# Performance work log

Measured on AMD Instinct MI355X. Metric: run time of the kernel, lower is better.

Reference implementation:

```python
import jax, jax.numpy as jnp
import numpy as np

B, V, H, W, CIN, COUT = 2, 4, 256, 256, 64, 64
WINDOW = 1
GAMMA = 0.1


def setup_inputs() -> dict:
    key = jax.random.key(0)
    ks = jax.random.split(key, 6)
    # gaussian positions: x,y in [-1,1], z in [0.5,2.5] so projection masks are nontrivial
    means = jax.random.uniform(ks[0], (B, V, H, W, 3), dtype=jnp.float32)
    means = means * jnp.array([2.0, 2.0, 2.0], jnp.float32) + jnp.array([-1.0, -1.0, 0.5], jnp.float32)
    depths = jax.random.uniform(ks[1], (B, V, H, W, 1, 1), dtype=jnp.float32)
    gs_feats = jax.random.normal(ks[2], (B, V, H, W, CIN), dtype=jnp.float32)
    # normalized intrinsics (ndc in [0,1))
    intr = jnp.array([[0.8, 0.0, 0.5], [0.0, 0.8, 0.5], [0.0, 0.0, 1.0]], jnp.float32)
    intrinsics = jnp.broadcast_to(intr, (B, V, 3, 3))
    # camera-to-world extrinsics: identity rotation, small per-view translations
    t = jax.random.uniform(ks[3], (B, V, 3), minval=-0.2, maxval=0.2, dtype=jnp.float32)
    extrinsics = jnp.broadcast_to(jnp.eye(4, dtype=jnp.float32), (B, V, 4, 4)).at[..., :3, 3].set(t)
    w1 = jax.random.normal(ks[4], (COUT, CIN, 3, 3), dtype=jnp.float32) * 0.05
    b1 = jnp.zeros((COUT,), jnp.float32)
    w2 = jax.random.normal(ks[5], (COUT, COUT, 3, 3), dtype=jnp.float32) * 0.05
    b2 = jnp.zeros((COUT,), jnp.float32)
    return {"means": means, "depths": depths, "gs_feats": gs_feats,
            "intrinsics": intrinsics, "extrinsics": extrinsics,
            "w1": w1, "b1": b1, "w2": w2, "b2": b2}


def _project(points, intr, extr, eps=1e-8):
    # points (b, n, 3) world; extr (b,4,4) cam-to-world; intr (b,3,3) normalized
    w2c = jnp.linalg.inv(extr)
    ph = jnp.concatenate([points, jnp.ones_like(points[..., :1])], axis=-1)  # (b,n,4)
    cam = jnp.einsum('bij,bnj->bni', w2c, ph)[..., :3]
    z = cam[..., 2:3]
    ndc = jnp.einsum('bij,bnj->bni', intr, cam / (z + eps))
    return ndc[..., :2], cam[..., 2] > eps


def _conv3x3(x, w, b):
    y = jax.lax.conv_general_dilated(x, w, (1, 1), 'SAME',
                                     dimension_numbers=('NCHW', 'OIHW', 'NCHW'))
    return y + b[None, :, None, None]


def reference(means, depths, gs_feats, intrinsics, extrinsics, w1, b1, w2, b2):
    b, v, h, w_, c = gs_feats.shape
    hw = h * w_
    feats_flat = gs_feats.reshape(b, v, hw, c)
    pts = means.reshape(b, v, hw, 3)
    outs = []
    for j in range(v):
        acc = feats_flat[:, j]                      # (b, hw, c)
        norm = jnp.ones((b,), gs_feats.dtype)
        for k in range(v):
            if j != k and (k - WINDOW) <= j <= (k + WINDOW):
                ndc, valid_z = _project(pts[:, j], intrinsics[:, k], extrinsics[:, k])
                px = jnp.floor(ndc[..., 0] * w_).astype(jnp.int32)
                py = jnp.floor(ndc[..., 1] * h).astype(jnp.int32)
                mask = ((ndc[..., 0] >= 0) & (ndc[..., 0] < 1) &
                        (ndc[..., 1] >= 0) & (ndc[..., 1] < 1) & valid_z)  # (b,hw)
                idx = jnp.clip(py, 0, h - 1) * w_ + jnp.clip(px, 0, w_ - 1)
                gathered = jnp.take_along_axis(feats_flat[:, k], idx[..., None], axis=1)
                upd = jnp.where(mask[..., None], gathered, jnp.zeros((), gs_feats.dtype))
                scale = GAMMA * mask.sum(-1).astype(gs_feats.dtype) / (h * w_)  # (b,)
                acc = acc + upd * scale[:, None, None]
                norm = norm + scale
        outs.append(acc / norm[:, None, None])
    fused = jnp.stack(outs, axis=1).reshape(b * v, h, w_, c).transpose(0, 3, 1, 2)  # (bv,c,h,w)
    x = _conv3x3(fused, w1, b1)
    x = jax.nn.gelu(x, approximate=False)
    x = _conv3x3(x, w2, b2)
    return x.transpose(0, 2, 3, 1).reshape(b, v, h, w_, -1)
```

## Files before the change

kernel.cpp:

```cpp
#include <hip/hip_runtime.h>
#include <math.h>

#define HW 65536
#define NPAD 258

typedef short bf16x8 __attribute__((ext_vector_type(8)));
typedef float f32x4  __attribute__((ext_vector_type(4)));

#define O_COUNTS 0
#define O_W2C    2048
#define O_WT     4096
#define O_META   151552
#define O_FUSED  3297280
#define O_X1     71458816

#define HROWB   4224
#define HROWSTR 4240
#define HBUF    25440

__device__ __forceinline__ unsigned short f2bf(float f) {
    unsigned int u = __float_as_uint(f);
    u += 0x7FFFu + ((u >> 16) & 1u);
    return (unsigned short)(u >> 16);
}

__device__ __forceinline__ unsigned int cvt_pk_bf16(float lo, float hi) {
    unsigned int r;
    asm("v_cvt_pk_bf16_f32 %0, %1, %2" : "=v"(r) : "v"(lo), "v"(hi));
    return r;
}

__device__ __forceinline__ float gelu_fast(float v) {
    float x  = v * 0.70710678118654752f;
    float ax = fabsf(x);
    float t  = __builtin_amdgcn_rcpf(fmaf(0.3275911f, ax, 1.0f));
    float p  = fmaf(t, 1.061405429f, -1.453152027f);
    p = fmaf(t, p, 1.421413741f);
    p = fmaf(t, p, -0.284496736f);
    p = fmaf(t, p, 0.254829592f);
    p = p * t;
    float e   = __expf(-x * x);
    float era = fmaf(-p, e, 1.0f);
    float er  = copysignf(era, x);
    return 0.5f * v * (1.0f + er);
}

__global__ __launch_bounds__(256) void prep_kernel(
    const float* __restrict__ extr, const float* __restrict__ w1,
    const float* __restrict__ w2, float* __restrict__ w2c,
    unsigned short* __restrict__ wT, unsigned short* __restrict__ fusedP,
    unsigned short* __restrict__ x1P, int* __restrict__ counts)
{
    int tid = blockIdx.x * blockDim.x + threadIdx.x;
    int nth = gridDim.x * blockDim.x;

    if (blockIdx.x == 0) {
        if (threadIdx.x < 8) {
            float a[4][8];
            const float* E = extr + threadIdx.x * 16;
            for (int r = 0; r < 4; r++)
                for (int c = 0; c < 4; c++) {
                    a[r][c] = E[r*4 + c];
                    a[r][4+c] = (r == c) ? 1.0f : 0.0f;
                }
            for (int col = 0; col < 4; col++) {
                int piv = col; float bm = fabsf(a[col][col]);
                for (int r = col+1; r < 4; r++) {
                    float v = fabsf(a[r][col]);
                    if (v > bm) { bm = v; piv = r; }
                }
                if (piv != col)
                    for (int c = 0; c < 8; c++) { float t = a[col][c]; a[col][c] = a[piv][c]; a[piv][c] = t; }
                float f = 1.0f / a[col][col];
                for (int c = 0; c < 8; c++) a[col][c] *= f;
                for (int r = 0; r < 4; r++) if (r != col) {
                    float f2 = a[r][col];
                    for (int c = 0; c < 8; c++) a[r][c] -= f2 * a[col][c];
                }
            }
            float* O = w2c + threadIdx.x * 16;
            for (int r = 0; r < 4; r++)
                for (int c = 0; c < 4; c++) O[r*4+c] = a[r][4+c];
        }
    }

    for (int i = tid; i < 384; i += nth) counts[i] = 0;

    for (int e = tid; e < 73728; e += nth) {
        int t = e;
        int j  = t & 7;  t >>= 3;
        int co = t & 63; t >>= 6;
        int q  = t & 3;  t >>= 2;
        int tap = t % 9; t /= 9;
        int h  = t & 1;  int cv = t >> 1;
        int ci = h*32 + q*8 + j;
        int ky = tap / 3, kx = tap % 3;
        const float* wsrc = cv ? w2 : w1;
        float v = wsrc[((co*64 + ci)*3 + ky)*3 + kx];
        wT[cv*36864 + ((((h*9 + tap)*4 + q)*64 + co)*8 + j)] = f2bf(v);
    }

    for (int u = tid; u < 2*8*1028*8; u += nth) {
        int t = u;
        int ch   = t & 7;    t >>= 3;
        int cell = t % 1028; t /= 1028;
        int n    = t & 7;    int buf = t >> 3;
        int y, x;
        if      (cell < 258) { y = 0;   x = cell; }
        else if (cell < 516) { y = 257; x = cell - 258; }
        else if (cell < 772) { y = cell - 516 + 1; x = 0; }
        else                 { y = cell - 772 + 1; x = 257; }
        unsigned short* p = (buf ? x1P : fusedP) +
            (((size_t)(n*NPAD + y)*NPAD + x)*64 + ch*8);
        *reinterpret_cast<uint4*>(p) = make_uint4(0u, 0u, 0u, 0u);
    }
}

__global__ __launch_bounds__(256) void proj_kernel(
    const float* __restrict__ means, const float* __restrict__ intr,
    const float* __restrict__ w2c, int* __restrict__ meta,
    int* __restrict__ counts)
{
    const int jt[6] = {0,1,1,2,2,3};
    const int kt[6] = {1,0,2,1,3,2};
    int s = blockIdx.y;
    int b = s / 6, p = s % 6;
    int j = jt[p], k = kt[p];
    int i = blockIdx.x * 256 + threadIdx.x;

    __shared__ int bcnt;
    if (threadIdx.x == 0) bcnt = 0;
    __syncthreads();

    const float* mp = means + ((size_t)(b*4 + j)*HW + i)*3;
    float x = mp[0], y = mp[1], z = mp[2];
    const float* M = w2c + (b*4 + k)*16;
    const float* I = intr + (b*4 + k)*9;

    float cx = fmaf(M[2],  z, fmaf(M[1], y, M[0]*x)) + M[3];
    float cy = fmaf(M[6],  z, fmaf(M[5], y, M[4]*x)) + M[7];
    float cz = fmaf(M[10], z, fmaf(M[9], y, M[8]*x)) + M[11];

    bool vz = cz > 1e-8f;
    float zi = cz + 1e-8f;
    float sx = cx / zi, sy = cy / zi, sz = cz / zi;
    float nx = fmaf(I[2], sz, fmaf(I[1], sy, I[0]*sx));
    float ny = fmaf(I[5], sz, fmaf(I[4], sy, I[3]*sx));

    int px = (int)floorf(nx * 256.0f);
    int py = (int)floorf(ny * 256.0f);
    bool mask = (nx >= 0.0f) && (nx < 1.0f) && (ny >= 0.0f) && (ny < 1.0f) && vz;
    int pxc = min(max(px, 0), 255);
    int pyc = min(max(py, 0), 255);
    int idx = pyc*256 + pxc;
    meta[(size_t)s*HW + i] = idx | (mask ? (int)0x80000000 : 0);

    unsigned long long bal = __ballot(mask ? 1 : 0);
    if ((threadIdx.x & 63) == 0)
        atomicAdd(&bcnt, (int)__popcll(bal));
    __syncthreads();
    if (threadIdx.x == 0)
        atomicAdd(counts + s*32, bcnt);
}

__global__ __launch_bounds__(256) void fuse_kernel(
    const float* __restrict__ feats, const int* __restrict__ meta,
    const int* __restrict__ counts, unsigned short* __restrict__ fusedP)
{
    const int nsl[4]    = {1, 2, 2, 1};
    const int slt[4][2] = {{0,0},{1,2},{3,4},{5,5}};
    const int kvw[4][2] = {{1,1},{0,2},{1,3},{2,2}};

    int bj = blockIdx.y;
    int b = bj >> 2, j = bj & 3;
    int base = blockIdx.x * 32;
    int cg = threadIdx.x & 15;
    int pt0 = base + (threadIdx.x >> 4);
    int pt1 = pt0 + 16;

    int ns = nsl[j];

    const float4* fj0 = reinterpret_cast<const float4*>(
        feats + ((size_t)bj*HW + pt0)*64) + cg;
    const float4* fj1 = reinterpret_cast<const float4*>(
        feats + ((size_t)bj*HW + pt1)*64) + cg;
    float4 acc0 = *fj0;
    float4 acc1 = *fj1;
    float norm = 1.0f;

#pragma unroll
    for (int e = 0; e < 2; e++) {
        if (e < ns) {
            int p = slt[j][e], k = kvw[j][e];
            int s = b*6 + p;
            float scale = 0.1f * (float)counts[s*32] / 65536.0f;
            int mt0 = meta[(size_t)s*HW + pt0];
            int mt1 = meta[(size_t)s*HW + pt1];
            const float* fk = feats + (size_t)(b*4 + k)*HW*64;
            float4 g0 = *(reinterpret_cast<const float4*>(
                fk + (size_t)(mt0 & 0xFFFF)*64) + cg);
            float4 g1 = *(reinterpret_cast<const float4*>(
                fk + (size_t)(mt1 & 0xFFFF)*64) + cg);
            float w0 = (mt0 < 0) ? scale : 0.0f;
            float w1 = (mt1 < 0) ? scale : 0.0f;
            acc0.x = fmaf(w0, g0.x, acc0.x); acc0.y = fmaf(w0, g0.y, acc0.y);
            acc0.z = fmaf(w0, g0.z, acc0.z); acc0.w = fmaf(w0, g0.w, acc0.w);
            acc1.x = fmaf(w1, g1.x, acc1.x); acc1.y = fmaf(w1, g1.y, acc1.y);
            acc1.z = fmaf(w1, g1.z, acc1.z); acc1.w = fmaf(w1, g1.w, acc1.w);
            norm += scale;
        }
    }
    float rn = 1.0f / norm;

    int yy0 = pt0 >> 8, xx0 = pt0 & 255;
    unsigned short* op0 = fusedP +
        (((size_t)bj*NPAD + (yy0+1))*NPAD + (xx0+1))*64 + cg*4;
    *reinterpret_cast<uint2*>(op0) =
        make_uint2(cvt_pk_bf16(acc0.x*rn, acc0.y*rn),
                   cvt_pk_bf16(acc0.z*rn, acc0.w*rn));

    int yy1 = pt1 >> 8, xx1 = pt1 & 255;
    unsigned short* op1 = fusedP +
        (((size_t)bj*NPAD + (yy1+1))*NPAD + (xx1+1))*64 + cg*4;
    *reinterpret_cast<uint2*>(op1) =
        make_uint2(cvt_pk_bf16(acc1.x*rn, acc1.y*rn),
                   cvt_pk_bf16(acc1.z*rn, acc1.w*rn));
}

template<int MODE>
__global__ __launch_bounds__(256) void conv_kernel(
    const unsigned short* __restrict__ in, const unsigned short* __restrict__ wT,
    const float* __restrict__ bias, void* __restrict__ outp)
{
    __shared__ unsigned short smem[2 * HBUF / 2];

    int fid = blockIdx.x;
    int n   = fid & 7;
    int rem = fid >> 3;
    int y0  = (rem >> 2) << 2;
    int X0  = (rem & 3) << 6;

    int w  = threadIdx.x >> 6;
    int lane = threadIdx.x & 63;
    int m = lane & 15, q = lane >> 4;

    int srcl = ((lane >> 2) * 128) + ((((lane & 3) ^ ((lane >> 3) & 3)) & 3) << 4);
    int tsrcl = 8192 + ((lane >> 2) * 128) + ((lane & 3) << 4);

    int vb[3];
#pragma unroll
    for (int dx = 0; dx < 3; dx++)
        vb[dx] = w*HROWSTR + m*64 + (((q ^ (((m + dx) >> 1) & 3)) & 3) << 4);

    int wvoff = q*1024 + m*16;

    const char* gb00 = (const char*)in +
        (((size_t)(n*NPAD) + y0) * NPAD + X0) * 128;

    auto STAGE = [&](int row128, int h, int buf) {
        const char* gb = gb00 + (size_t)row128 * (NPAD*128) + h*64;
        char* lb = (char*)smem + buf*HBUF;
        for (int ri = w; ri < 6; ri += 4) {
            const char* g = gb + (size_t)ri * (NPAD*128);
            char* l = lb + ri*HROWSTR;
#pragma unroll
            for (int i = 0; i < 4; i++)
                __builtin_amdgcn_global_load_lds(
                    (const __attribute__((address_space(1))) unsigned int*)(g + i*2048 + srcl),
                    (__attribute__((address_space(3))) unsigned int*)(l + i*1024 + (size_t)lane*16),
                    16, 0, 0);
            if (lane < 8)
                __builtin_amdgcn_global_load_lds(
                    (const __attribute__((address_space(1))) unsigned int*)(g + tsrcl),
                    (__attribute__((address_space(3))) unsigned int*)(l + 4096 + (size_t)lane*16),
                    16, 0, 0);
        }
    };

    f32x4 acc[4][4];
    auto ACCZERO = [&]() {
#pragma unroll
        for (int a = 0; a < 4; a++)
#pragma unroll
            for (int bq = 0; bq < 4; bq++)
                acc[a][bq] = (f32x4){0.f, 0.f, 0.f, 0.f};
    };

    auto COMPUTE = [&](int h, int buf) {
        const char* sb = (const char*)smem + buf*HBUF;
        const char* wbase = (const char*)wT + h*36864;
        __builtin_amdgcn_s_setprio(1);
#pragma unroll
        for (int tap = 0; tap < 9; tap++) {
            int dy = tap/3, dx = tap%3;
            const char* wtap = wbase + tap*4096;
            bf16x8 av[4], bv[4];
#pragma unroll
            for (int Mt = 0; Mt < 4; Mt++)
                av[Mt] = *reinterpret_cast<const bf16x8*>(
                    sb + vb[dx] + dy*HROWSTR + Mt*1024 + dx*64);
#pragma unroll
            for (int Nt = 0; Nt < 4; Nt++)
                bv[Nt] = *reinterpret_cast<const bf16x8*>(wtap + wvoff + Nt*256);
#pragma unroll
            for (int Mt = 0; Mt < 4; Mt++)
#pragma unroll
                for (int Nt = 0; Nt < 4; Nt++)
                    acc[Mt][Nt] = __builtin_amdgcn_mfma_f32_16x16x32_bf16(
                        bv[Nt], av[Mt], acc[Mt][Nt], 0, 0, 0);
        }
        __builtin_amdgcn_s_setprio(0);
    };

    auto EPI = [&](int row128) {
        int yout = y0 + row128 + w;
        float4 bsv[4];
#pragma unroll
        for (int Nt = 0; Nt < 4; Nt++)
            bsv[Nt] = *reinterpret_cast<const float4*>(bias + Nt*16 + q*4);
        if (MODE == 1) {
            char* obase = (char*)outp +
                (((size_t)(n*NPAD + yout + 1))*NPAD + (X0 + 1))*128 + m*128 + q*8;
#pragma unroll
            for (int Mt = 0; Mt < 4; Mt++) {
                char* ob = obase + Mt*2048;
#pragma unroll
                for (int Nt = 0; Nt < 4; Nt++) {
                    float v0 = gelu_fast(acc[Mt][Nt][0] + bsv[Nt].x);
                    float v1 = gelu_fast(acc[Mt][Nt][1] + bsv[Nt].y);
                    float v2 = gelu_fast(acc[Mt][Nt][2] + bsv[Nt].z);
                    float v3 = gelu_fast(acc[Mt][Nt][3] + bsv[Nt].w);
                    uint2 pk = make_uint2(cvt_pk_bf16(v0, v1), cvt_pk_bf16(v2, v3));
                    *reinterpret_cast<uint2*>(ob + Nt*32) = pk;
                }
            }
        } else {
            char* obase = (char*)outp +
                (((size_t)(n*256 + yout))*256 + X0)*256 + m*256 + q*16;
#pragma unroll
            for (int Mt = 0; Mt < 4; Mt++) {
                char* ob = obase + Mt*4096;
#pragma unroll
                for (int Nt = 0; Nt < 4; Nt++) {
                    float4 v = make_float4(acc[Mt][Nt][0] + bsv[Nt].x,
                                           acc[Mt][Nt][1] + bsv[Nt].y,
                                           acc[Mt][Nt][2] + bsv[Nt].z,
                                           acc[Mt][Nt][3] + bsv[Nt].w);
                    *reinterpret_cast<float4*>(ob + Nt*64) = v;
                }
            }
        }
    };

    ACCZERO();
    STAGE(0, 0, 0);
    __syncthreads();

    STAGE(0, 1, 1);
    COMPUTE(0, 0);
    __syncthreads();

    STAGE(128, 0, 0);
    COMPUTE(1, 1);
    EPI(0);
    ACCZERO();
    __syncthreads();

    STAGE(128, 1, 1);
    COMPUTE(0, 0);
    __syncthreads();

    COMPUTE(1, 1);
    EPI(128);
}

extern "C" void kernel_launch(void* const* d_in, const int* in_sizes, int n_in,
                              void* d_out, int out_size, void* d_ws, size_t ws_size,
                              hipStream_t stream)
{
    const float* means = (const float*)d_in[0];
    const float* feats = (const float*)d_in[2];
    const float* intr  = (const float*)d_in[3];
    const float* extr  = (const float*)d_in[4];
    const float* w1    = (const float*)d_in[5];
    const float* b1    = (const float*)d_in[6];
    const float* w2    = (const float*)d_in[7];
    const float* b2    = (const float*)d_in[8];

    char* ws = (char*)d_ws;
    int*            counts = (int*)(ws + O_COUNTS);
    float*          w2c    = (float*)(ws + O_W2C);
    unsigned short* wT     = (unsigned short*)(ws + O_WT);
    int*            meta   = (int*)(ws + O_META);
    unsigned short* fusedP = (unsigned short*)(ws + O_FUSED);
    unsigned short* x1P    = (unsigned short*)(ws + O_X1);

    prep_kernel<<<dim3(96), dim3(256), 0, stream>>>(
        extr, w1, w2, w2c, wT, fusedP, x1P, counts);
    proj_kernel<<<dim3(256, 12), dim3(256), 0, stream>>>(
        means, intr, w2c, meta, counts);
    fuse_kernel<<<dim3(2048, 8), dim3(256), 0, stream>>>(
        feats, meta, counts, fusedP);
    conv_kernel<1><<<dim3(1024), dim3(256), 0, stream>>>(
        fusedP, wT, b1, (void*)x1P);
    conv_kernel<2><<<dim3(1024), dim3(256), 0, stream>>>(
        x1P, wT + 36864, b2, d_out);
}
```

Baseline: 376.1 us.

## Stage conv weights in LDS and split output channels across 8 waves

The conv kernel goes from 256 to 512 threads. The 8 waves split into 4 row waves times 2 output-channel halves, so each wave holds only 4x2 accumulators. Weights for each input-channel half are now copied into LDS by waves 6 and 7 rather than read per tap from global memory, and the pixel tile is single-buffered with extra barriers, replacing the previous double-buffered overlap. This aims to cut redundant global weight traffic and register pressure to raise occupancy, at the cost of losing load/compute overlap and adding more synchronization.

```diff
diff --git a/kernel.cpp b/kernel.cpp
--- a/kernel.cpp
+++ b/kernel.cpp
@@ -16,7 +16,8 @@
 
 #define HROWB   4224
 #define HROWSTR 4240
-#define HBUF    25440
+#define PXBUF   25440
+#define WBUF    36864
 
 __device__ __forceinline__ unsigned short f2bf(float f) {
     unsigned int u = __float_as_uint(f);
@@ -228,11 +229,12 @@
 }
 
 template<int MODE>
-__global__ __launch_bounds__(256) void conv_kernel(
+__global__ __launch_bounds__(512) void conv_kernel(
     const unsigned short* __restrict__ in, const unsigned short* __restrict__ wT,
     const float* __restrict__ bias, void* __restrict__ outp)
 {
-    __shared__ unsigned short smem[2 * HBUF / 2];
+    __shared__ unsigned short smem[(PXBUF + WBUF) / 2];
+    unsigned short* wlds = smem + PXBUF/2;
 
     int fid = blockIdx.x;
     int n   = fid & 7;
@@ -240,7 +242,9 @@
     int y0  = (rem >> 2) << 2;
     int X0  = (rem & 3) << 6;
 
-    int w  = threadIdx.x >> 6;
+    int w    = threadIdx.x >> 6;
+    int row  = w & 3;
+    int cH   = w >> 2;
     int lane = threadIdx.x & 63;
     int m = lane & 15, q = lane >> 4;
 
@@ -250,19 +254,18 @@
     int vb[3];
 #pragma unroll
     for (int dx = 0; dx < 3; dx++)
-        vb[dx] = w*HROWSTR + m*64 + (((q ^ (((m + dx) >> 1) & 3)) & 3) << 4);
+        vb[dx] = row*HROWSTR + m*64 + (((q ^ (((m + dx) >> 1) & 3)) & 3) << 4);
 
     int wvoff = q*1024 + m*16;
 
     const char* gb00 = (const char*)in +
         (((size_t)(n*NPAD) + y0) * NPAD + X0) * 128;
 
-    auto STAGE = [&](int row128, int h, int buf) {
-        const char* gb = gb00 + (size_t)row128 * (NPAD*128) + h*64;
-        char* lb = (char*)smem + buf*HBUF;
-        for (int ri = w; ri < 6; ri += 4) {
-            const char* g = gb + (size_t)ri * (NPAD*128);
-            char* l = lb + ri*HROWSTR;
+    auto STAGE_PX = [&](int row128, int h) {
+        if (w < 6) {
+            const char* g = gb00 + (size_t)row128 * (NPAD*128) + h*64
+                          + (size_t)w * (NPAD*128);
+            char* l = (char*)smem + w*HROWSTR;
 #pragma unroll
             for (int i = 0; i < 4; i++)
                 __builtin_amdgcn_global_load_lds(
@@ -277,55 +280,69 @@
         }
     };
 
-    f32x4 acc[4][4];
-    auto ACCZERO = [&]() {
-#pragma unroll
-        for (int a = 0; a < 4; a++)
-#pragma unroll
-            for (int bq = 0; bq < 4; bq++)
-                acc[a][bq] = (f32x4){0.f, 0.f, 0.f, 0.f};
+    auto STAGE_W = [&](int h) {
+        const char* wh = (const char*)wT + h*36864 + wvoff;
+        char* ld = (char*)wlds + (size_t)lane*16;
+        if (w == 6) {
+#pragma unroll
+            for (int tap = 0; tap < 4; tap++)
+#pragma unroll
+                for (int i = 0; i < 4; i++)
+                    __builtin_amdgcn_global_load_lds(
+                        (const __attribute__((address_space(1))) unsigned int*)(wh + tap*4096 + i*256),
+                        (__attribute__((address_space(3))) unsigned int*)(ld + tap*4096 + i*1024),
+                        16, 0, 0);
+        } else if (w == 7) {
+#pragma unroll
+            for (int tap = 4; tap < 9; tap++)
+#pragma unroll
+                for (int i = 0; i < 4; i++)
+                    __builtin_amdgcn_global_load_lds(
+                        (const __attribute__((address_space(1))) unsigned int*)(wh + tap*4096 + i*256),
+                        (__attribute__((address_space(3))) unsigned int*)(ld + tap*4096 + i*1024),
+                        16, 0, 0);
+        }
     };
 
-    auto COMPUTE = [&](int h, int buf) {
-        const char* sb = (const char*)smem + buf*HBUF;
-        const char* wbase = (const char*)wT + h*36864;
+    auto COMPUTE = [&](f32x4 (&acc)[4][2]) {
+        const char* sb = (const char*)smem;
+        const char* wb = (const char*)wlds + (size_t)lane*16 + cH*2048;
         __builtin_amdgcn_s_setprio(1);
 #pragma unroll
         for (int tap = 0; tap < 9; tap++) {
             int dy = tap/3, dx = tap%3;
-            const char* wtap = wbase + tap*4096;
-            bf16x8 av[4], bv[4];
+            bf16x8 av[4], bv[2];
 #pragma unroll
             for (int Mt = 0; Mt < 4; Mt++)
                 av[Mt] = *reinterpret_cast<const bf16x8*>(
                     sb + vb[dx] + dy*HROWSTR + Mt*1024 + dx*64);
 #pragma unroll
-            for (int Nt = 0; Nt < 4; Nt++)
-                bv[Nt] = *reinterpret_cast<const bf16x8*>(wtap + wvoff + Nt*256);
+            for (int Nt = 0; Nt < 2; Nt++)
+                bv[Nt] = *reinterpret_cast<const bf16x8*>(wb + tap*4096 + Nt*1024);
 #pragma unroll
             for (int Mt = 0; Mt < 4; Mt++)
 #pragma unroll
-                for (int Nt = 0; Nt < 4; Nt++)
+                for (int Nt = 0; Nt < 2; Nt++)
                     acc[Mt][Nt] = __builtin_amdgcn_mfma_f32_16x16x32_bf16(
                         bv[Nt], av[Mt], acc[Mt][Nt], 0, 0, 0);
         }
         __builtin_amdgcn_s_setprio(0);
     };
 
-    auto EPI = [&](int row128) {
-        int yout = y0 + row128 + w;
-        float4 bsv[4];
-#pragma unroll
-        for (int Nt = 0; Nt < 4; Nt++)
-            bsv[Nt] = *reinterpret_cast<const float4*>(bias + Nt*16 + q*4);
+    auto EPI = [&](int row128, f32x4 (&acc)[4][2]) {
+        int yout = y0 + row128 + row;
+        float4 bsv[2];
+#pragma unroll
+        for (int Nt = 0; Nt < 2; Nt++)
+            bsv[Nt] = *reinterpret_cast<const float4*>(bias + cH*32 + Nt*16 + q*4);
         if (MODE == 1) {
             char* obase = (char*)outp +
-                (((size_t)(n*NPAD + yout + 1))*NPAD + (X0 + 1))*128 + m*128 + q*8;
+                (((size_t)(n*NPAD + yout + 1))*NPAD + (X0 + 1))*128 + m*128 + q*8 + cH*64;
 #pragma unroll
             for (int Mt = 0; Mt < 4; Mt++) {
                 char* ob = obase + Mt*2048;
 #pragma unroll
-                for (int Nt = 0; Nt < 4; Nt++) {
+                for (int Nt = 0; Nt < 2; Nt++) {
                     float v0 = gelu_fast(acc[Mt][Nt][0] + bsv[Nt].x);
                     float v1 = gelu_fast(acc[Mt][Nt][1] + bsv[Nt].y);
                     float v2 = gelu_fast(acc[Mt][Nt][2] + bsv[Nt].z);
@@ -336,12 +353,12 @@
             }
         } else {
             char* obase = (char*)outp +
-                (((size_t)(n*256 + yout))*256 + X0)*256 + m*256 + q*16;
+                (((size_t)(n*256 + yout))*256 + X0)*256 + m*256 + q*16 + cH*128;
 #pragma unroll
             for (int Mt = 0; Mt < 4; Mt++) {
                 char* ob = obase + Mt*4096;
 #pragma unroll
-                for (int Nt = 0; Nt < 4; Nt++) {
+                for (int Nt = 0; Nt < 2; Nt++) {
                     float4 v = make_float4(acc[Mt][Nt][0] + bsv[Nt].x,
                                            acc[Mt][Nt][1] + bsv[Nt].y,
                                            acc[Mt][Nt][2] + bsv[Nt].z,
@@ -352,26 +369,39 @@
         }
     };
 
-    ACCZERO();
-    STAGE(0, 0, 0);
-    __syncthreads();
-
-    STAGE(0, 1, 1);
-    COMPUTE(0, 0);
-    __syncthreads();
-
-    STAGE(128, 0, 0);
-    COMPUTE(1, 1);
-    EPI(0);
-    ACCZERO();
-    __syncthreads();
-
-    STAGE(128, 1, 1);
-    COMPUTE(0, 0);
-    __syncthreads();
-
-    COMPUTE(1, 1);
-    EPI(128);
+    f32x4 accA[4][2], accB[4][2];
+#pragma unroll
+    for (int a = 0; a < 4; a++)
+#pragma unroll
+        for (int bq = 0; bq < 2; bq++) {
+            accA[a][bq] = (f32x4){0.f, 0.f, 0.f, 0.f};
+            accB[a][bq] = (f32x4){0.f, 0.f, 0.f, 0.f};
+        }
+
+    STAGE_W(0); STAGE_PX(0, 0);
+    __syncthreads();
+
+    COMPUTE(accA);
+    __syncthreads();
+
+    STAGE_PX(128, 0);
+    __syncthreads();
+
+    COMPUTE(accB);
+    __syncthreads();
+
+    STAGE_W(1); STAGE_PX(0, 1);
+    __syncthreads();
+
+    COMPUTE(accA);
+    __syncthreads();
+
+    STAGE_PX(128, 1);
+    EPI(0, accA);
+    __syncthreads();
+
+    COMPUTE(accB);
+    EPI(128, accB);
 }
 
 extern "C" void kernel_launch(void* const* d_in, const int* in_sizes, int n_in,
@@ -401,8 +431,8 @@
         means, intr, w2c, meta, counts);
     fuse_kernel<<<dim3(2048, 8), dim3(256), 0, stream>>>(
         feats, meta, counts, fusedP);
-    conv_kernel<1><<<dim3(1024), dim3(256), 0, stream>>>(
+    conv_kernel<1><<<dim3(1024), dim3(512), 0, stream>>>(
         fusedP, wT, b1, (void*)x1P);
-    conv_kernel<2><<<dim3(1024), dim3(256), 0, stream>>>(
+    conv_kernel<2><<<dim3(1024), dim3(512), 0, stream>>>(
         x1P, wT + 36864, b2, d_out);
 }
```

Measured after the change: 355.6 us. -5.4%, faster.
